# Optimization experiments

Hardware: AMD Instinct MI355X
Metric: run time of the kernel (lower is better)

Reference implementation:

```python
import jax, jax.numpy as jnp
import numpy as np

P = 3; C = 64; IMG = 48; G = IMG // P
D = C * P * P          # 576 embedding dim == flatten dim
NH = 12; HD = D // NH  # 48 head dim
HID = 4 * D            # 2304
NL = 4; S = G * G      # 256 patches
NQ = 6
QN, QP = -8.0, 7.0     # 4-bit signed LSQ range
EPS = 1e-5


def lsq(w):
    # LSQ fake-quant of weights, step size from LSQ init formula, STE rounding
    alpha = 2.0 * jnp.mean(jnp.abs(w)) / jnp.sqrt(QP)
    q = jnp.clip(w / alpha, QN, QP)
    q = q + jax.lax.stop_gradient(jnp.round(q) - q)
    return q * alpha


def qlinear(x, w, b=None):
    y = x @ lsq(w).T
    return y if b is None else y + b


def ln(x, g, b):
    m = jnp.mean(x, -1, keepdims=True)
    v = jnp.var(x, -1, keepdims=True)
    return (x - m) / jnp.sqrt(v + EPS) * g + b


def mha(q, k, v, in_w, out_w):
    # q,k,v: [S,B,D]; in_w: [3D,D]; out_w: [D,D]; no biases
    Wq, Wk, Wv = jnp.split(lsq(in_w), 3, axis=0)
    def heads(t, W):
        return (t @ W.T).reshape(t.shape[0], t.shape[1], NH, HD)
    qh = heads(q, Wq) * (1.0 / jnp.sqrt(HD))
    kh = heads(k, Wk)
    vh = heads(v, Wv)
    att = jax.nn.softmax(jnp.einsum('qbhd,kbhd->bhqk', qh, kh), axis=-1)
    o = jnp.einsum('bhqk,kbhd->qbhd', att, vh).reshape(q.shape[0], q.shape[1], D)
    return o @ lsq(out_w).T


def _forward(x, lin_enc_w, lin_enc_b, pos_emb, query_embed_w,
             enc_in_w, enc_out_w, enc_l1_w, enc_l1_b, enc_l2_w, enc_l2_b,
             enc_ln1_g, enc_ln1_b, enc_ln2_g, enc_ln2_b,
             dec_sa_in_w, dec_sa_out_w, dec_ca_in_w, dec_ca_out_w,
             dec_l1_w, dec_l1_b, dec_l2_w, dec_l2_b,
             dec_ln1_g, dec_ln1_b, dec_ln2_g, dec_ln2_b, dec_ln3_g, dec_ln3_b,
             head1_w, head1_b, head2_w, head2_b, query_idx):
    B = x.shape[0]
    # unfold -> [S,B,flat], channel-major patch flattening like F.unfold
    t = x.reshape(B, C, G, P, G, P).transpose(0, 1, 3, 5, 2, 4)
    t = t.reshape(B, C * P * P, G * G).transpose(2, 0, 1)  # [S,B,D]
    t = qlinear(t, lin_enc_w, lin_enc_b) + t
    qe = query_embed_w[query_idx].reshape(S, 1, D)   # query_pos, broadcasts over B
    pos = pos_emb[:, None, :]                        # [S,1,D]
    h = t + pos
    for l in range(NL):  # encoder (pre-norm)
        h2 = ln(h, enc_ln1_g[l], enc_ln1_b[l])
        h = h + mha(h2, h2, h2, enc_in_w[l], enc_out_w[l])
        h2 = ln(h, enc_ln2_g[l], enc_ln2_b[l])
        h = h + qlinear(jax.nn.relu(qlinear(h2, enc_l1_w[l], enc_l1_b[l])), enc_l2_w[l], enc_l2_b[l])
    mem = h
    o = mem
    for l in range(NL):  # decoder, memory = encoder output
        o2 = ln(o, dec_ln1_g[l], dec_ln1_b[l])
        qk = o2 + qe
        o = o + mha(qk, qk, o2, dec_sa_in_w[l], dec_sa_out_w[l])
        o2 = ln(o, dec_ln2_g[l], dec_ln2_b[l])
        o = o + mha(o2 + qe, mem, mem, dec_ca_in_w[l], dec_ca_out_w[l])
        o2 = ln(o, dec_ln3_g[l], dec_ln3_b[l])
        o = o + qlinear(jax.nn.relu(qlinear(o2, dec_l1_w[l], dec_l1_b[l])), dec_l2_w[l], dec_l2_b[l])
    # mlp_head with residual
    o = o + qlinear(jax.nn.relu(qlinear(o, head1_w, head1_b)), head2_w, head2_b)
    # fold back: [S,B,D] -> [B,C,IMG,IMG]
    y = o.transpose(1, 2, 0).reshape(B, C, P, P, G, G).transpose(0, 1, 4, 2, 5, 3)
    return y.reshape(B, C, IMG, IMG)


def setup_inputs() -> dict:
    key = jax.random.key(0)
    ks = iter(jax.random.split(key, 64))
    def w(shape):
        return jax.random.normal(next(ks), shape, jnp.float32) * 0.02
    B = 4
    inp = {
        'x': jax.random.normal(next(ks), (B, C, IMG, IMG), jnp.float32),
        'lin_enc_w': w((D, D)), 'lin_enc_b': jnp.zeros((D,), jnp.float32),
        'pos_emb': w((S, D)),
        'query_embed_w': w((NQ, S * D)),
        'enc_in_w': w((NL, 3 * D, D)), 'enc_out_w': w((NL, D, D)),
        'enc_l1_w': w((NL, HID, D)), 'enc_l1_b': jnp.zeros((NL, HID), jnp.float32),
        'enc_l2_w': w((NL, D, HID)), 'enc_l2_b': jnp.zeros((NL, D), jnp.float32),
        'enc_ln1_g': jnp.ones((NL, D), jnp.float32), 'enc_ln1_b': jnp.zeros((NL, D), jnp.float32),
        'enc_ln2_g': jnp.ones((NL, D), jnp.float32), 'enc_ln2_b': jnp.zeros((NL, D), jnp.float32),
        'dec_sa_in_w': w((NL, 3 * D, D)), 'dec_sa_out_w': w((NL, D, D)),
        'dec_ca_in_w': w((NL, 3 * D, D)), 'dec_ca_out_w': w((NL, D, D)),
        'dec_l1_w': w((NL, HID, D)), 'dec_l1_b': jnp.zeros((NL, HID), jnp.float32),
        'dec_l2_w': w((NL, D, HID)), 'dec_l2_b': jnp.zeros((NL, D), jnp.float32),
        'dec_ln1_g': jnp.ones((NL, D), jnp.float32), 'dec_ln1_b': jnp.zeros((NL, D), jnp.float32),
        'dec_ln2_g': jnp.ones((NL, D), jnp.float32), 'dec_ln2_b': jnp.zeros((NL, D), jnp.float32),
        'dec_ln3_g': jnp.ones((NL, D), jnp.float32), 'dec_ln3_b': jnp.zeros((NL, D), jnp.float32),
        'head1_w': w((HID, D)), 'head1_b': jnp.zeros((HID,), jnp.float32),
        'head2_w': w((D, HID)), 'head2_b': jnp.zeros((D,), jnp.float32),
        'query_idx': 0,
    }
    return inp


def reference(x, lin_enc_w, lin_enc_b, pos_emb, query_embed_w,
              enc_in_w, enc_out_w, enc_l1_w, enc_l1_b, enc_l2_w, enc_l2_b,
              enc_ln1_g, enc_ln1_b, enc_ln2_g, enc_ln2_b,
              dec_sa_in_w, dec_sa_out_w, dec_ca_in_w, dec_ca_out_w,
              dec_l1_w, dec_l1_b, dec_l2_w, dec_l2_b,
              dec_ln1_g, dec_ln1_b, dec_ln2_g, dec_ln2_b, dec_ln3_g, dec_ln3_b,
              head1_w, head1_b, head2_w, head2_b, query_idx):
    return _forward(x, lin_enc_w, lin_enc_b, pos_emb, query_embed_w,
                    enc_in_w, enc_out_w, enc_l1_w, enc_l1_b, enc_l2_w, enc_l2_b,
                    enc_ln1_g, enc_ln1_b, enc_ln2_g, enc_ln2_b,
                    dec_sa_in_w, dec_sa_out_w, dec_ca_in_w, dec_ca_out_w,
                    dec_l1_w, dec_l1_b, dec_l2_w, dec_l2_b,
                    dec_ln1_g, dec_ln1_b, dec_ln2_g, dec_ln2_b, dec_ln3_g, dec_ln3_b,
                    head1_w, head1_b, head2_w, head2_b, query_idx)
```

## Files before the change

kernel.cpp:

```cpp
#include <hip/hip_runtime.h>
#include <cstddef>

#define Pp    3
#define Cc    64
#define IMGi  48
#define Gg    16
#define Dd    576
#define NHh   12
#define HDd   48
#define HIDh  2304
#define NLl   4
#define Ss    256
#define Bb    4
#define Mm    1024
#define EPSf  1e-5f
#define NJOBS 43
#define NSTAT 20

typedef short short8 __attribute__((ext_vector_type(8)));
typedef short short4v __attribute__((ext_vector_type(4)));
typedef float f32x4  __attribute__((ext_vector_type(4)));
typedef unsigned short ushort_t;

struct QJobs { const float* ptr[NJOBS]; int n[NJOBS]; int off[NJOBS]; };

__device__ __forceinline__ short f2bf(float f) {
  unsigned u = __float_as_uint(f);
  u = u + 0x7fffu + ((u >> 16) & 1u);
  return (short)(u >> 16);
}
__device__ __forceinline__ float bf2f(short s) {
  return __uint_as_float(((unsigned)(unsigned short)s) << 16);
}

typedef __attribute__((address_space(3))) unsigned lds_u32;
typedef __attribute__((address_space(1))) const unsigned glob_u32;
__device__ __forceinline__ void gload_lds16(const void* g, void* l) {
  __builtin_amdgcn_global_load_lds((glob_u32*)g, (lds_u32*)l, 16, 0, 0);
}


__global__ void k_zero(float* p, int n) {
  int i = blockIdx.x * blockDim.x + threadIdx.x;
  if (i < n) p[i] = 0.f;
}

__global__ void k_abssum(QJobs jobs, float* absum) {
  int job = blockIdx.x >> 6, blk = blockIdx.x & 63;
  const float4* p4 = (const float4*)jobs.ptr[job];
  int n4 = jobs.n[job] >> 2;
  float s0 = 0.f, s1 = 0.f, s2 = 0.f, s3 = 0.f;
  for (int i = blk * 1024 + threadIdx.x; i < n4; i += 64 * 1024) {
    float4 v = p4[i];
    s0 += fabsf(v.x) + fabsf(v.y) + fabsf(v.z) + fabsf(v.w);
    int i1 = i + 256;
    if (i1 < n4) { float4 w = p4[i1]; s1 += fabsf(w.x) + fabsf(w.y) + fabsf(w.z) + fabsf(w.w); }
    int i2 = i + 512;
    if (i2 < n4) { float4 w = p4[i2]; s2 += fabsf(w.x) + fabsf(w.y) + fabsf(w.z) + fabsf(w.w); }
    int i3 = i + 768;
    if (i3 < n4) { float4 w = p4[i3]; s3 += fabsf(w.x) + fabsf(w.y) + fabsf(w.z) + fabsf(w.w); }
  }
  float s = (s0 + s1) + (s2 + s3);
  #pragma unroll
  for (int o = 32; o; o >>= 1) s += __shfl_xor(s, o);
  __shared__ float red[4];
  if ((threadIdx.x & 63) == 0) red[threadIdx.x >> 6] = s;
  __syncthreads();
  if (threadIdx.x == 0) atomicAdd(&absum[job], (red[0] + red[1]) + (red[2] + red[3]));
}

__global__ void k_alpha(QJobs jobs, const float* absum, float* alpha, float* inva) {
  int j = threadIdx.x;
  if (j < NJOBS) {
    float a = 2.f * (absum[j] / (float)jobs.n[j]) / sqrtf(7.f);
    alpha[j] = a;
    inva[j] = 1.f / a;
  }
}

__global__ void k_quant(QJobs jobs, const float* __restrict__ inva, short* __restrict__ wq) {
  int job = blockIdx.x >> 7, blk = blockIdx.x & 127;
  const float* p = jobs.ptr[job];
  int n8 = jobs.n[job] >> 3;
  short* dst = wq + (size_t)jobs.off[job];
  float ia = inva[job];
  for (int i = blk * 512 + threadIdx.x; i < n8; i += 128 * 512) {
    const float4* p4 = (const float4*)(p + (size_t)i * 8);
    float4 w0 = p4[0], w1 = p4[1];
    int i1 = i + 256;
    float4 w2, w3;
    bool has2 = i1 < n8;
    if (has2) { const float4* q4 = (const float4*)(p + (size_t)i1 * 8); w2 = q4[0]; w3 = q4[1]; }
    short8 bv;
    bv[0] = f2bf(rintf(fminf(7.f, fmaxf(-8.f, w0.x * ia))));
    bv[1] = f2bf(rintf(fminf(7.f, fmaxf(-8.f, w0.y * ia))));
    bv[2] = f2bf(rintf(fminf(7.f, fmaxf(-8.f, w0.z * ia))));
    bv[3] = f2bf(rintf(fminf(7.f, fmaxf(-8.f, w0.w * ia))));
    bv[4] = f2bf(rintf(fminf(7.f, fmaxf(-8.f, w1.x * ia))));
    bv[5] = f2bf(rintf(fminf(7.f, fmaxf(-8.f, w1.y * ia))));
    bv[6] = f2bf(rintf(fminf(7.f, fmaxf(-8.f, w1.z * ia))));
    bv[7] = f2bf(rintf(fminf(7.f, fmaxf(-8.f, w1.w * ia))));
    *(short8*)(dst + (size_t)i * 8) = bv;
    if (has2) {
      short8 cv;
      cv[0] = f2bf(rintf(fminf(7.f, fmaxf(-8.f, w2.x * ia))));
      cv[1] = f2bf(rintf(fminf(7.f, fmaxf(-8.f, w2.y * ia))));
      cv[2] = f2bf(rintf(fminf(7.f, fmaxf(-8.f, w2.z * ia))));
      cv[3] = f2bf(rintf(fminf(7.f, fmaxf(-8.f, w2.w * ia))));
      cv[4] = f2bf(rintf(fminf(7.f, fmaxf(-8.f, w3.x * ia))));
      cv[5] = f2bf(rintf(fminf(7.f, fmaxf(-8.f, w3.y * ia))));
      cv[6] = f2bf(rintf(fminf(7.f, fmaxf(-8.f, w3.z * ia))));
      cv[7] = f2bf(rintf(fminf(7.f, fmaxf(-8.f, w3.w * ia))));
      *(short8*)(dst + (size_t)i1 * 8) = cv;
    }
  }
}

__global__ void k_patchify(const float* __restrict__ x, float* __restrict__ t,
                           ushort_t* __restrict__ tb) {
  int i = blockIdx.x * 256 + threadIdx.x;
  if (i >= Mm * Dd) return;
  int d = i % Dd, row = i / Dd;
  int b = row % Bb, s = row / Bb;
  int c = d / 9, r = d % 9;
  int p1 = r / 3, p2 = r % 3;
  int g1 = s / Gg, g2 = s % Gg;
  float v = x[((size_t)(b * Cc + c) * IMGi + (g1 * Pp + p1)) * IMGi + (g2 * Pp + p2)];
  t[i] = v;
  tb[i] = (ushort_t)f2bf(v);
}

__global__ void k_unpatch(const float* __restrict__ h, float* __restrict__ out) {
  int i = blockIdx.x * 256 + threadIdx.x;
  if (i >= Bb * Cc * IMGi * IMGi) return;
  int j = i % IMGi, t = i / IMGi;
  int r = t % IMGi; t /= IMGi;
  int c = t % Cc;
  int b = t / Cc;
  int g1 = r / Pp, p1 = r % Pp, g2 = j / Pp, p2 = j % Pp;
  int s = g1 * Gg + g2;
  int d = c * 9 + p1 * 3 + p2;
  out[i] = h[(size_t)(s * Bb + b) * Dd + d];
}

#define MT 64
#define NT 64
#define KC 288
#define LDKB 304
#define BCHUNKS 38

__device__ __forceinline__ int bswz(int row, int colByte) {
  return row * (LDKB * 2) + (colByte ^ (((row >> 2) & 3) << 4));
}

__device__ __forceinline__ void stage_async(const ushort_t* base, int ld,
                                            char* lds, int wave, int lane) {
  #pragma unroll
  for (int j = 0; j < 10; ++j) {
    const int c = wave * 10 + j;
    if (c < BCHUNKS) {
      const int p = c * 512 + lane * 8;
      const int prow = p / LDKB;
      const int pcol2 = (p % LDKB) * 2;
      const int lcol = pcol2 ^ (((prow >> 2) & 3) << 4);
      const ushort_t* src = (lcol < 576)
        ? base + (size_t)prow * ld + (lcol >> 1)
        : base;
      gload_lds16(src, lds + c * 1024);
    }
  }
}

__global__ __launch_bounds__(256)
void k_gemm_mfma(const ushort_t* __restrict__ Xa, const ushort_t* __restrict__ Xb,
                 int n_split, int ldx,
                 const float* __restrict__ qe, const int* __restrict__ qidx,
                 const float* __restrict__ lng, const float* __restrict__ lnb,
                 const float* __restrict__ statA, const float* __restrict__ statB,
                 const float* __restrict__ Wraw, const short* __restrict__ Wq,
                 const float* __restrict__ bias, const float* __restrict__ pos,
                 const float* res, int ldr,
                 float* out, int ldo,
                 ushort_t* outbf, ushort_t* outbf2, float* statOut,
                 int N, int K,
                 const float* __restrict__ alpha_p, const float* __restrict__ inva_p,
                 int slot, int relu)
{
  __shared__ short As[NT * LDKB];
  __shared__ short Bs[NT * LDKB];
  const int tid  = threadIdx.x;
  const int wave = tid >> 6, lane = tid & 63;
  const int quad = lane >> 4, l15 = lane & 15;
  const int tile_m = blockIdx.y * MT, tile_n = blockIdx.x * NT;
  const int m_off = (wave >> 1) * 32, n_off = (wave & 1) * 32;
  const int sr = tid >> 2;
  const int sc = (tid & 3) * 8;
  const float inva = inva_p[slot];

  const bool isA = (!Xb || tile_n < n_split);
  const ushort_t* X = isA ? Xa : Xb;
  const bool addqe = (qe != nullptr) && isA;
  const float* stat = isA ? statA : statB;
  const bool a_reg = (stat != nullptr) || addqe;
  size_t qe_off = 0;
  if (addqe) qe_off = (size_t)qidx[0] * ((size_t)Ss * Dd);

  float mean = 0.f, sinv = 1.f;
  if (stat) {
    float2 st = *(const float2*)&stat[2 * (tile_m + sr)];
    mean = st.x * (1.f / (float)Dd);
    float var = st.y * (1.f / (float)Dd) - mean * mean;
    sinv = rsqrtf(var + EPSf);
  }

  f32x4 acc00 = {0,0,0,0}, acc01 = {0,0,0,0}, acc10 = {0,0,0,0}, acc11 = {0,0,0,0};

  for (int kc = 0; kc < K; kc += KC) {
    if (Wq) {
      stage_async((const ushort_t*)Wq + (size_t)tile_n * K + kc, K,
                  (char*)Bs, wave, lane);
    } else {
      const float* wr = Wraw + (size_t)(tile_n + sr) * K + kc;
      #pragma unroll
      for (int j = 0; j < 9; ++j) {
        const int k = sc + j * 32;
        float4 w0 = *(const float4*)(wr + k);
        float4 w1 = *(const float4*)(wr + k + 4);
        short8 bv;
        bv[0] = f2bf(rintf(fminf(7.f, fmaxf(-8.f, w0.x * inva))));
        bv[1] = f2bf(rintf(fminf(7.f, fmaxf(-8.f, w0.y * inva))));
        bv[2] = f2bf(rintf(fminf(7.f, fmaxf(-8.f, w0.z * inva))));
        bv[3] = f2bf(rintf(fminf(7.f, fmaxf(-8.f, w0.w * inva))));
        bv[4] = f2bf(rintf(fminf(7.f, fmaxf(-8.f, w1.x * inva))));
        bv[5] = f2bf(rintf(fminf(7.f, fmaxf(-8.f, w1.y * inva))));
        bv[6] = f2bf(rintf(fminf(7.f, fmaxf(-8.f, w1.z * inva))));
        bv[7] = f2bf(rintf(fminf(7.f, fmaxf(-8.f, w1.w * inva))));
        *(short8*)((char*)Bs + bswz(sr, k * 2)) = bv;
      }
    }

    if (!a_reg) {
      stage_async(X + (size_t)tile_m * ldx + kc, ldx, (char*)As, wave, lane);
    } else {
      const int arow = tile_m + sr;
      const ushort_t* xr = X + (size_t)arow * ldx + kc;
      const float* qr = addqe ? (qe + qe_off + (size_t)(arow >> 2) * Dd + kc) : nullptr;
      #pragma unroll
      for (int j = 0; j < 9; ++j) {
        const int k = sc + j * 32;
        short8 xv = *(const short8*)(xr + k);
        float a[8];
        #pragma unroll
        for (int e = 0; e < 8; ++e) a[e] = bf2f(xv[e]);
        if (stat) {
          float4 g0 = *(const float4*)(lng + kc + k);
          float4 g1 = *(const float4*)(lng + kc + k + 4);
          float4 b0 = *(const float4*)(lnb + kc + k);
          float4 b1 = *(const float4*)(lnb + kc + k + 4);
          a[0] = (a[0] - mean) * sinv * g0.x + b0.x;
          a[1] = (a[1] - mean) * sinv * g0.y + b0.y;
          a[2] = (a[2] - mean) * sinv * g0.z + b0.z;
          a[3] = (a[3] - mean) * sinv * g0.w + b0.w;
          a[4] = (a[4] - mean) * sinv * g1.x + b1.x;
          a[5] = (a[5] - mean) * sinv * g1.y + b1.y;
          a[6] = (a[6] - mean) * sinv * g1.z + b1.z;
          a[7] = (a[7] - mean) * sinv * g1.w + b1.w;
        }
        if (addqe) {
          float4 q0 = *(const float4*)(qr + k);
          float4 q1 = *(const float4*)(qr + k + 4);
          a[0] += q0.x; a[1] += q0.y; a[2] += q0.z; a[3] += q0.w;
          a[4] += q1.x; a[5] += q1.y; a[6] += q1.z; a[7] += q1.w;
        }
        short8 av;
        #pragma unroll
        for (int e = 0; e < 8; ++e) av[e] = f2bf(a[e]);
        *(short8*)((char*)As + bswz(sr, k * 2)) = av;
      }
    }
    __syncthreads();

    #pragma unroll 3
    for (int ks = 0; ks < KC / 32; ++ks) {
      const int kb = ks * 32 + quad * 8;
      short8 af0 = *(const short8*)((const char*)As + bswz(m_off + l15, kb * 2));
      short8 af1 = *(const short8*)((const char*)As + bswz(m_off + 16 + l15, kb * 2));
      short8 bf0 = *(const short8*)((const char*)Bs + bswz(n_off + l15, kb * 2));
      short8 bf1 = *(const short8*)((const char*)Bs + bswz(n_off + 16 + l15, kb * 2));
      acc00 = __builtin_amdgcn_mfma_f32_16x16x32_bf16(af0, bf0, acc00, 0, 0, 0);
      acc01 = __builtin_amdgcn_mfma_f32_16x16x32_bf16(af0, bf1, acc01, 0, 0, 0);
      acc10 = __builtin_amdgcn_mfma_f32_16x16x32_bf16(af1, bf0, acc10, 0, 0, 0);
      acc11 = __builtin_amdgcn_mfma_f32_16x16x32_bf16(af1, bf1, acc11, 0, 0, 0);
    }
    __syncthreads();
  }

  const float a_s = alpha_p[slot];
  const int rowb = tile_m + m_off + quad * 4;
  const int colb = tile_n + n_off + l15;
  f32x4 accs[4] = {acc00, acc01, acc10, acc11};
  float vsum[2][4], vsq[2][4];
  #pragma unroll
  for (int rt = 0; rt < 2; ++rt)
    #pragma unroll
    for (int r = 0; r < 4; ++r) { vsum[rt][r] = 0.f; vsq[rt][r] = 0.f; }

  #pragma unroll
  for (int t = 0; t < 4; ++t) {
    int row0 = rowb + ((t >> 1) * 16);
    int col  = colb + ((t & 1) * 16);
    float bv = bias ? bias[col] : 0.f;
    #pragma unroll
    for (int r = 0; r < 4; ++r) {
      int row = row0 + r;
      float v = accs[t][r] * a_s + bv;
      if (res) v += res[(size_t)row * ldr + col];
      if (pos) v += pos[(size_t)(row >> 2) * Dd + col];
      if (relu) v = fmaxf(v, 0.f);
      if (out)    out[(size_t)row * ldo + col] = v;
      if (outbf)  outbf[(size_t)row * ldo + col]  = (ushort_t)f2bf(v);
      if (outbf2) outbf2[(size_t)row * ldo + col] = (ushort_t)f2bf(v);
      vsum[t >> 1][r] += v;
      vsq[t >> 1][r]  += v * v;
    }
  }

  if (statOut) {
    #pragma unroll
    for (int rt = 0; rt < 2; ++rt) {
      #pragma unroll
      for (int r = 0; r < 4; ++r) {
        float s = vsum[rt][r], q = vsq[rt][r];
        #pragma unroll
        for (int o = 1; o < 16; o <<= 1) {
          s += __shfl_xor(s, o);
          q += __shfl_xor(q, o);
        }
        if (l15 == 0) {
          int row = rowb + rt * 16 + r;
          atomicAdd(&statOut[2 * row],     s);
          atomicAdd(&statOut[2 * row + 1], q);
        }
      }
    }
  }
}

__global__ __launch_bounds__(256)
void k_attn(const ushort_t* __restrict__ QKV, ushort_t* __restrict__ ctx, float scale) {
  __shared__ short Ks[256][72];
  __shared__ short Qs[64][72];
  __shared__ short Vt[48][264];
  __shared__ short Pq[64][264];
  const int qt = blockIdx.x;
  const int b  = blockIdx.y / NHh, h = blockIdx.y % NHh;
  const int tid = threadIdx.x;
  const int w = tid >> 6, lane = tid & 63, quad = lane >> 4, l15 = lane & 15;

  {
    const ushort_t* kp = QKV + (size_t)(tid * Bb + b) * 1728 + Dd + h * HDd;
    #pragma unroll
    for (int d0 = 0; d0 < 48; d0 += 8)
      *(short8*)&Ks[tid][d0] = *(const short8*)(kp + d0);
    short4v z = {0, 0, 0, 0};
    *(short4v*)&Ks[tid][48] = z; *(short4v*)&Ks[tid][52] = z;
    *(short4v*)&Ks[tid][56] = z; *(short4v*)&Ks[tid][60] = z;
    const ushort_t* vp = QKV + (size_t)(tid * Bb + b) * 1728 + 2 * Dd + h * HDd;
    #pragma unroll
    for (int d0 = 0; d0 < 48; d0 += 8) {
      short8 v = *(const short8*)(vp + d0);
      #pragma unroll
      for (int e = 0; e < 8; ++e) Vt[d0 + e][tid] = v[e];
    }
    if (tid < 64) {
      const ushort_t* qp = QKV + (size_t)((qt * 64 + tid) * Bb + b) * 1728 + h * HDd;
      #pragma unroll
      for (int d0 = 0; d0 < 48; d0 += 8)
        *(short8*)&Qs[tid][d0] = *(const short8*)(qp + d0);
      *(short4v*)&Qs[tid][48] = z; *(short4v*)&Qs[tid][52] = z;
      *(short4v*)&Qs[tid][56] = z; *(short4v*)&Qs[tid][60] = z;
    }
  }
  __syncthreads();

  short8 bq0 = *(short8*)&Qs[w * 16 + l15][quad * 8];
  short8 bq1 = *(short8*)&Qs[w * 16 + l15][32 + quad * 8];
  f32x4 sf[16];
  #pragma unroll
  for (int mt = 0; mt < 16; ++mt) {
    f32x4 acc = {0, 0, 0, 0};
    short8 a0 = *(short8*)&Ks[mt * 16 + l15][quad * 8];
    short8 a1 = *(short8*)&Ks[mt * 16 + l15][32 + quad * 8];
    acc = __builtin_amdgcn_mfma_f32_16x16x32_bf16(a0, bq0, acc, 0, 0, 0);
    acc = __builtin_amdgcn_mfma_f32_16x16x32_bf16(a1, bq1, acc, 0, 0, 0);
    sf[mt] = acc;
  }

  float mx = -1e30f;
  #pragma unroll
  for (int mt = 0; mt < 16; ++mt)
    #pragma unroll
    for (int r = 0; r < 4; ++r) {
      sf[mt][r] *= scale;
      mx = fmaxf(mx, sf[mt][r]);
    }
  mx = fmaxf(mx, __shfl_xor(mx, 16));
  mx = fmaxf(mx, __shfl_xor(mx, 32));
  float sum = 0.f;
  #pragma unroll
  for (int mt = 0; mt < 16; ++mt)
    #pragma unroll
    for (int r = 0; r < 4; ++r) {
      float e = __expf(sf[mt][r] - mx);
      sf[mt][r] = e;
      sum += e;
    }
  sum += __shfl_xor(sum, 16);
  sum += __shfl_xor(sum, 32);
  float inv = 1.f / sum;

  #pragma unroll
  for (int mt = 0; mt < 16; ++mt) {
    short4v p = { f2bf(sf[mt][0] * inv), f2bf(sf[mt][1] * inv),
                  f2bf(sf[mt][2] * inv), f2bf(sf[mt][3] * inv) };
    *(short4v*)&Pq[w * 16 + l15][mt * 16 + quad * 4] = p;
  }
  __syncthreads();

  f32x4 of0 = {0,0,0,0}, of1 = {0,0,0,0}, of2 = {0,0,0,0};
  #pragma unroll
  for (int kt = 0; kt < 8; ++kt) {
    short8 a = *(short8*)&Pq[w * 16 + l15][kt * 32 + quad * 8];
    short8 b0 = *(short8*)&Vt[l15][kt * 32 + quad * 8];
    short8 b1 = *(short8*)&Vt[16 + l15][kt * 32 + quad * 8];
    short8 b2 = *(short8*)&Vt[32 + l15][kt * 32 + quad * 8];
    of0 = __builtin_amdgcn_mfma_f32_16x16x32_bf16(a, b0, of0, 0, 0, 0);
    of1 = __builtin_amdgcn_mfma_f32_16x16x32_bf16(a, b1, of1, 0, 0, 0);
    of2 = __builtin_amdgcn_mfma_f32_16x16x32_bf16(a, b2, of2, 0, 0, 0);
  }
  const int qg = qt * 64 + w * 16 + quad * 4;
  #pragma unroll
  for (int r = 0; r < 4; ++r) {
    ushort_t* cr = ctx + (size_t)((qg + r) * Bb + b) * Dd + h * HDd + l15;
    cr[0]  = (ushort_t)f2bf(of0[r]);
    cr[16] = (ushort_t)f2bf(of1[r]);
    cr[32] = (ushort_t)f2bf(of2[r]);
  }
}


extern "C" void kernel_launch(void* const* d_in, const int* in_sizes, int n_in,
                              void* d_out, int out_size, void* d_ws, size_t ws_size,
                              hipStream_t stream) {
  (void)in_sizes; (void)n_in; (void)out_size;
  const float* x            = (const float*)d_in[0];
  const float* lin_enc_w    = (const float*)d_in[1];
  const float* lin_enc_b    = (const float*)d_in[2];
  const float* pos_emb      = (const float*)d_in[3];
  const float* query_embed  = (const float*)d_in[4];
  const float* enc_in_w     = (const float*)d_in[5];
  const float* enc_out_w    = (const float*)d_in[6];
  const float* enc_l1_w     = (const float*)d_in[7];
  const float* enc_l1_b     = (const float*)d_in[8];
  const float* enc_l2_w     = (const float*)d_in[9];
  const float* enc_l2_b     = (const float*)d_in[10];
  const float* enc_ln1_g    = (const float*)d_in[11];
  const float* enc_ln1_b    = (const float*)d_in[12];
  const float* enc_ln2_g    = (const float*)d_in[13];
  const float* enc_ln2_b    = (const float*)d_in[14];
  const float* dec_sa_in_w  = (const float*)d_in[15];
  const float* dec_sa_out_w = (const float*)d_in[16];
  const float* dec_ca_in_w  = (const float*)d_in[17];
  const float* dec_ca_out_w = (const float*)d_in[18];
  const float* dec_l1_w     = (const float*)d_in[19];
  const float* dec_l1_b     = (const float*)d_in[20];
  const float* dec_l2_w     = (const float*)d_in[21];
  const float* dec_l2_b     = (const float*)d_in[22];
  const float* dec_ln1_g    = (const float*)d_in[23];
  const float* dec_ln1_b    = (const float*)d_in[24];
  const float* dec_ln2_g    = (const float*)d_in[25];
  const float* dec_ln2_b    = (const float*)d_in[26];
  const float* dec_ln3_g    = (const float*)d_in[27];
  const float* dec_ln3_b    = (const float*)d_in[28];
  const float* head1_w      = (const float*)d_in[29];
  const float* head1_b      = (const float*)d_in[30];
  const float* head2_w      = (const float*)d_in[31];
  const float* head2_b      = (const float*)d_in[32];
  const int*   query_idx    = (const int*)d_in[33];
  float* out = (float*)d_out;

  const int DD  = Dd * Dd;
  const int IN3 = 3 * Dd * Dd;
  const int FF  = HIDh * Dd;
  const int MD  = Mm * Dd;

  float* ws = (float*)d_ws;
  float* ABSUM = ws;
  float* ALPHA = ws + 64;
  float* INVA  = ws + 128;
  float* STAT  = ws + 256;
  const int STATF = NSTAT * Mm * 2;
  float* H   = STAT + STATF;
  float* SCR = H + MD;
  ushort_t* Hb   = (ushort_t*)(SCR + MD);
  ushort_t* SCRb = Hb + MD;
  ushort_t* MEMb = SCRb + MD;
  ushort_t* CTXb = MEMb + MD;
  ushort_t* QKVb = CTXb + MD;
  size_t act_bytes = (256 + (size_t)STATF + 2 * (size_t)MD) * 4
                   + (4 * (size_t)MD + (size_t)Mm * HIDh) * 2;
  short* WQ = (short*)(QKVb + (size_t)Mm * HIDh);
  const size_t WQ_ELEMS = (size_t)DD + 4 * ((size_t)IN3 + DD + FF + FF)
                        + 4 * ((size_t)IN3 + DD + IN3 + DD + FF + FF)
                        + 2 * (size_t)FF;
  const bool use_wq = ws_size >= act_bytes + WQ_ELEMS * 2;

  auto T = [&](int i) { return STAT + (size_t)i * (Mm * 2); };

  QJobs jobs;
  int j = 0; int off = 0;
  auto addjob = [&](const float* p, int n) { jobs.ptr[j] = p; jobs.n[j] = n; jobs.off[j] = off; off += n; j++; };
  addjob(lin_enc_w, DD);
  for (int l = 0; l < NLl; ++l) addjob(enc_in_w  + (size_t)l * IN3, IN3);
  for (int l = 0; l < NLl; ++l) addjob(enc_out_w + (size_t)l * DD,  DD);
  for (int l = 0; l < NLl; ++l) addjob(enc_l1_w  + (size_t)l * FF,  FF);
  for (int l = 0; l < NLl; ++l) addjob(enc_l2_w  + (size_t)l * FF,  FF);
  for (int l = 0; l < NLl; ++l) addjob(dec_sa_in_w  + (size_t)l * IN3, IN3);
  for (int l = 0; l < NLl; ++l) addjob(dec_sa_out_w + (size_t)l * DD,  DD);
  for (int l = 0; l < NLl; ++l) addjob(dec_ca_in_w  + (size_t)l * IN3, IN3);
  for (int l = 0; l < NLl; ++l) addjob(dec_ca_out_w + (size_t)l * DD,  DD);
  for (int l = 0; l < NLl; ++l) addjob(dec_l1_w + (size_t)l * FF, FF);
  for (int l = 0; l < NLl; ++l) addjob(dec_l2_w + (size_t)l * FF, FF);
  addjob(head1_w, FF);
  addjob(head2_w, FF);

  const int ZN = 256 + STATF;
  k_zero<<<(ZN + 255) / 256, 256, 0, stream>>>(ws, ZN);
  k_abssum<<<NJOBS * 64, 256, 0, stream>>>(jobs, ABSUM);
  k_alpha<<<1, 64, 0, stream>>>(jobs, ABSUM, ALPHA, INVA);
  if (use_wq) k_quant<<<NJOBS * 128, 256, 0, stream>>>(jobs, INVA, WQ);

  auto gemm = [&](const ushort_t* Xa, const ushort_t* Xb, int n_split, int ldx,
                  const float* qe, const float* lng, const float* lnb,
                  const float* statA, const float* statB,
                  const float* W, int slot, const float* bias, const float* pos,
                  const float* res, int ldr,
                  float* o, int ldo, ushort_t* obf, ushort_t* obf2,
                  float* statOut, int N, int K, int relu) {
    dim3 grid(N / NT, Mm / MT);
    const short* wq = use_wq ? WQ + (size_t)jobs.off[slot] : nullptr;
    const float* wr = use_wq ? nullptr : W;
    k_gemm_mfma<<<grid, 256, 0, stream>>>(Xa, Xb, n_split, ldx, qe, query_idx,
                                          lng, lnb, statA, statB,
                                          wr, wq, bias, pos, res, ldr,
                                          o, ldo, obf, obf2, statOut,
                                          N, K, ALPHA, INVA, slot, relu);
  };

  const float scale = 1.f / sqrtf((float)HDd);
  auto attn = [&](const float* out_w, int out_slot, float* statOut) {
    k_attn<<<dim3(Ss / 64, Bb * NHh), 256, 0, stream>>>(QKVb, CTXb, scale);
    gemm(CTXb, nullptr, 0, Dd, nullptr, nullptr, nullptr, nullptr, nullptr,
         out_w, out_slot, nullptr, nullptr, H, Dd,
         H, Dd, Hb, nullptr, statOut, Dd, Dd, 0);
  };

  const int NELEM = Mm * Dd;
  const int EB = (NELEM + 255) / 256;

  k_patchify<<<EB, 256, 0, stream>>>(x, SCR, SCRb);
  gemm(SCRb, nullptr, 0, Dd, nullptr, nullptr, nullptr, nullptr, nullptr,
       lin_enc_w, 0, lin_enc_b, pos_emb, SCR, Dd,
       H, Dd, Hb, nullptr, T(0), Dd, Dd, 0);

  for (int l = 0; l < NLl; ++l) {
    gemm(Hb, nullptr, 0, Dd, nullptr, enc_ln1_g + l * Dd, enc_ln1_b + l * Dd,
         T(2 * l), nullptr,
         enc_in_w + (size_t)l * IN3, 1 + l,
         nullptr, nullptr, nullptr, 0,
         nullptr, 1728, QKVb, nullptr, nullptr, 1728, Dd, 0);
    attn(enc_out_w + (size_t)l * DD, 5 + l, T(2 * l + 1));
    gemm(Hb, nullptr, 0, Dd, nullptr, enc_ln2_g + l * Dd, enc_ln2_b + l * Dd,
         T(2 * l + 1), nullptr,
         enc_l1_w + (size_t)l * FF, 9 + l,
         enc_l1_b + l * HIDh, nullptr, nullptr, 0,
         nullptr, HIDh, QKVb, nullptr, nullptr, HIDh, Dd, 1);
    gemm(QKVb, nullptr, 0, HIDh, nullptr, nullptr, nullptr, nullptr, nullptr,
         enc_l2_w + (size_t)l * FF, 13 + l,
         enc_l2_b + l * Dd, nullptr, H, Dd,
         H, Dd, Hb, (l == NLl - 1) ? MEMb : nullptr, T(2 * l + 2),
         Dd, HIDh, 0);
  }

  for (int l = 0; l < NLl; ++l) {
    float* ln1s = T(8 + 3 * l);
    gemm(Hb, Hb, 2 * Dd, Dd, query_embed,
         dec_ln1_g + l * Dd, dec_ln1_b + l * Dd, ln1s, ln1s,
         dec_sa_in_w + (size_t)l * IN3, 17 + l,
         nullptr, nullptr, nullptr, 0,
         nullptr, 1728, QKVb, nullptr, nullptr, 1728, Dd, 0);
    attn(dec_sa_out_w + (size_t)l * DD, 21 + l, T(9 + 3 * l));
    gemm(Hb, MEMb, Dd, Dd, query_embed,
         dec_ln2_g + l * Dd, dec_ln2_b + l * Dd, T(9 + 3 * l), nullptr,
         dec_ca_in_w + (size_t)l * IN3, 25 + l,
         nullptr, nullptr, nullptr, 0,
         nullptr, 1728, QKVb, nullptr, nullptr, 1728, Dd, 0);
    attn(dec_ca_out_w + (size_t)l * DD, 29 + l, T(10 + 3 * l));
    gemm(Hb, nullptr, 0, Dd, nullptr, dec_ln3_g + l * Dd, dec_ln3_b + l * Dd,
         T(10 + 3 * l), nullptr,
         dec_l1_w + (size_t)l * FF, 33 + l,
         dec_l1_b + l * HIDh, nullptr, nullptr, 0,
         nullptr, HIDh, QKVb, nullptr, nullptr, HIDh, Dd, 1);
    gemm(QKVb, nullptr, 0, HIDh, nullptr, nullptr, nullptr, nullptr, nullptr,
         dec_l2_w + (size_t)l * FF, 37 + l,
         dec_l2_b + l * Dd, nullptr, H, Dd,
         H, Dd, Hb, nullptr, (l < NLl - 1) ? T(11 + 3 * l) : nullptr,
         Dd, HIDh, 0);
  }

  gemm(Hb, nullptr, 0, Dd, nullptr, nullptr, nullptr, nullptr, nullptr,
       head1_w, 41, head1_b, nullptr, nullptr, 0,
       nullptr, HIDh, QKVb, nullptr, nullptr, HIDh, Dd, 1);
  gemm(QKVb, nullptr, 0, HIDh, nullptr, nullptr, nullptr, nullptr, nullptr,
       head2_w, 42, head2_b, nullptr, H, Dd,
       H, Dd, nullptr, nullptr, nullptr, Dd, HIDh, 0);

  k_unpatch<<<EB, 256, 0, stream>>>(H, out);
}
```

Baseline: 1.330 ms.

## Double-buffer GEMM LDS panels for large-K and widen weight-prep kernels

```diff
diff --git a/kernel.cpp b/kernel.cpp
--- a/kernel.cpp
+++ b/kernel.cpp
@@ -46,11 +46,11 @@
 }
 
 __global__ void k_abssum(QJobs jobs, float* absum) {
-  int job = blockIdx.x >> 6, blk = blockIdx.x & 63;
+  int job = blockIdx.x >> 7, blk = blockIdx.x & 127;
   const float4* p4 = (const float4*)jobs.ptr[job];
   int n4 = jobs.n[job] >> 2;
   float s0 = 0.f, s1 = 0.f, s2 = 0.f, s3 = 0.f;
-  for (int i = blk * 1024 + threadIdx.x; i < n4; i += 64 * 1024) {
+  for (int i = blk * 1024 + threadIdx.x; i < n4; i += 128 * 1024) {
     float4 v = p4[i];
     s0 += fabsf(v.x) + fabsf(v.y) + fabsf(v.z) + fabsf(v.w);
     int i1 = i + 256;
@@ -78,41 +78,35 @@
   }
 }
 
+__device__ __forceinline__ short8 quant8(const float* p, float ia) {
+  const float4* p4 = (const float4*)p;
+  float4 w0 = p4[0], w1 = p4[1];
+  short8 bv;
+  bv[0] = f2bf(rintf(fminf(7.f, fmaxf(-8.f, w0.x * ia))));
+  bv[1] = f2bf(rintf(fminf(7.f, fmaxf(-8.f, w0.y * ia))));
+  bv[2] = f2bf(rintf(fminf(7.f, fmaxf(-8.f, w0.z * ia))));
+  bv[3] = f2bf(rintf(fminf(7.f, fmaxf(-8.f, w0.w * ia))));
+  bv[4] = f2bf(rintf(fminf(7.f, fmaxf(-8.f, w1.x * ia))));
+  bv[5] = f2bf(rintf(fminf(7.f, fmaxf(-8.f, w1.y * ia))));
+  bv[6] = f2bf(rintf(fminf(7.f, fmaxf(-8.f, w1.z * ia))));
+  bv[7] = f2bf(rintf(fminf(7.f, fmaxf(-8.f, w1.w * ia))));
+  return bv;
+}
+
 __global__ void k_quant(QJobs jobs, const float* __restrict__ inva, short* __restrict__ wq) {
   int job = blockIdx.x >> 7, blk = blockIdx.x & 127;
   const float* p = jobs.ptr[job];
   int n8 = jobs.n[job] >> 3;
   short* dst = wq + (size_t)jobs.off[job];
   float ia = inva[job];
-  for (int i = blk * 512 + threadIdx.x; i < n8; i += 128 * 512) {
-    const float4* p4 = (const float4*)(p + (size_t)i * 8);
-    float4 w0 = p4[0], w1 = p4[1];
+  for (int i = blk * 1024 + threadIdx.x; i < n8; i += 128 * 1024) {
+    *(short8*)(dst + (size_t)i * 8) = quant8(p + (size_t)i * 8, ia);
     int i1 = i + 256;
-    float4 w2, w3;
-    bool has2 = i1 < n8;
-    if (has2) { const float4* q4 = (const float4*)(p + (size_t)i1 * 8); w2 = q4[0]; w3 = q4[1]; }
-    short8 bv;
-    bv[0] = f2bf(rintf(fminf(7.f, fmaxf(-8.f, w0.x * ia))));
-    bv[1] = f2bf(rintf(fminf(7.f, fmaxf(-8.f, w0.y * ia))));
-    bv[2] = f2bf(rintf(fminf(7.f, fmaxf(-8.f, w0.z * ia))));
-    bv[3] = f2bf(rintf(fminf(7.f, fmaxf(-8.f, w0.w * ia))));
-    bv[4] = f2bf(rintf(fminf(7.f, fmaxf(-8.f, w1.x * ia))));
-    bv[5] = f2bf(rintf(fminf(7.f, fmaxf(-8.f, w1.y * ia))));
-    bv[6] = f2bf(rintf(fminf(7.f, fmaxf(-8.f, w1.z * ia))));
-    bv[7] = f2bf(rintf(fminf(7.f, fmaxf(-8.f, w1.w * ia))));
-    *(short8*)(dst + (size_t)i * 8) = bv;
-    if (has2) {
-      short8 cv;
-      cv[0] = f2bf(rintf(fminf(7.f, fmaxf(-8.f, w2.x * ia))));
-      cv[1] = f2bf(rintf(fminf(7.f, fmaxf(-8.f, w2.y * ia))));
-      cv[2] = f2bf(rintf(fminf(7.f, fmaxf(-8.f, w2.z * ia))));
-      cv[3] = f2bf(rintf(fminf(7.f, fmaxf(-8.f, w2.w * ia))));
-      cv[4] = f2bf(rintf(fminf(7.f, fmaxf(-8.f, w3.x * ia))));
-      cv[5] = f2bf(rintf(fminf(7.f, fmaxf(-8.f, w3.y * ia))));
-      cv[6] = f2bf(rintf(fminf(7.f, fmaxf(-8.f, w3.z * ia))));
-      cv[7] = f2bf(rintf(fminf(7.f, fmaxf(-8.f, w3.w * ia))));
-      *(short8*)(dst + (size_t)i1 * 8) = cv;
-    }
+    if (i1 < n8) *(short8*)(dst + (size_t)i1 * 8) = quant8(p + (size_t)i1 * 8, ia);
+    int i2 = i + 512;
+    if (i2 < n8) *(short8*)(dst + (size_t)i2 * 8) = quant8(p + (size_t)i2 * 8, ia);
+    int i3 = i + 768;
+    if (i3 < n8) *(short8*)(dst + (size_t)i3 * 8) = quant8(p + (size_t)i3 * 8, ia);
   }
 }
 
@@ -147,6 +141,7 @@
 #define NT 64
 #define KC 288
 #define LDKB 304
+#define PANEL (NT * LDKB)
 #define BCHUNKS 38
 
 __device__ __forceinline__ int bswz(int row, int colByte) {
@@ -171,6 +166,7 @@
   }
 }
 
+template <int DB>
 __global__ __launch_bounds__(256)
 void k_gemm_mfma(const ushort_t* __restrict__ Xa, const ushort_t* __restrict__ Xb,
                  int n_split, int ldx,
@@ -186,8 +182,8 @@
                  const float* __restrict__ alpha_p, const float* __restrict__ inva_p,
                  int slot, int relu)
 {
-  __shared__ short As[NT * LDKB];
-  __shared__ short Bs[NT * LDKB];
+  __shared__ short As[DB * PANEL];
+  __shared__ short Bs[DB * PANEL];
   const int tid  = threadIdx.x;
   const int wave = tid >> 6, lane = tid & 63;
   const int quad = lane >> 4, l15 = lane & 15;
@@ -215,32 +211,24 @@
 
   f32x4 acc00 = {0,0,0,0}, acc01 = {0,0,0,0}, acc10 = {0,0,0,0}, acc11 = {0,0,0,0};
 
-  for (int kc = 0; kc < K; kc += KC) {
+  auto STAGE = [&](int kc, int buf) {
+    short* Asb = As + buf * PANEL;
+    short* Bsb = Bs + buf * PANEL;
     if (Wq) {
       stage_async((const ushort_t*)Wq + (size_t)tile_n * K + kc, K,
-                  (char*)Bs, wave, lane);
+                  (char*)Bsb, wave, lane);
     } else {
       const float* wr = Wraw + (size_t)(tile_n + sr) * K + kc;
       #pragma unroll
       for (int j = 0; j < 9; ++j) {
         const int k = sc + j * 32;
-        float4 w0 = *(const float4*)(wr + k);
-        float4 w1 = *(const float4*)(wr + k + 4);
         short8 bv;
-        bv[0] = f2bf(rintf(fminf(7.f, fmaxf(-8.f, w0.x * inva))));
-        bv[1] = f2bf(rintf(fminf(7.f, fmaxf(-8.f, w0.y * inva))));
-        bv[2] = f2bf(rintf(fminf(7.f, fmaxf(-8.f, w0.z * inva))));
-        bv[3] = f2bf(rintf(fminf(7.f, fmaxf(-8.f, w0.w * inva))));
-        bv[4] = f2bf(rintf(fminf(7.f, fmaxf(-8.f, w1.x * inva))));
-        bv[5] = f2bf(rintf(fminf(7.f, fmaxf(-8.f, w1.y * inva))));
-        bv[6] = f2bf(rintf(fminf(7.f, fmaxf(-8.f, w1.z * inva))));
-        bv[7] = f2bf(rintf(fminf(7.f, fmaxf(-8.f, w1.w * inva))));
-        *(short8*)((char*)Bs + bswz(sr, k * 2)) = bv;
+        bv = quant8(wr + k, inva);
+        *(short8*)((char*)Bsb + bswz(sr, k * 2)) = bv;
       }
     }
-
     if (!a_reg) {
-      stage_async(X + (size_t)tile_m * ldx + kc, ldx, (char*)As, wave, lane);
+      stage_async(X + (size_t)tile_m * ldx + kc, ldx, (char*)Asb, wave, lane);
     } else {
       const int arow = tile_m + sr;
       const ushort_t* xr = X + (size_t)arow * ldx + kc;
@@ -275,24 +263,44 @@
         short8 av;
         #pragma unroll
         for (int e = 0; e < 8; ++e) av[e] = f2bf(a[e]);
-        *(short8*)((char*)As + bswz(sr, k * 2)) = av;
+        *(short8*)((char*)Asb + bswz(sr, k * 2)) = av;
       }
     }
-    __syncthreads();
-
+  };
+
+  auto COMPUTE = [&](int buf) {
+    const short* Asb = As + buf * PANEL;
+    const short* Bsb = Bs + buf * PANEL;
     #pragma unroll 3
     for (int ks = 0; ks < KC / 32; ++ks) {
       const int kb = ks * 32 + quad * 8;
-      short8 af0 = *(const short8*)((const char*)As + bswz(m_off + l15, kb * 2));
-      short8 af1 = *(const short8*)((const char*)As + bswz(m_off + 16 + l15, kb * 2));
-      short8 bf0 = *(const short8*)((const char*)Bs + bswz(n_off + l15, kb * 2));
-      short8 bf1 = *(const short8*)((const char*)Bs + bswz(n_off + 16 + l15, kb * 2));
+      short8 af0 = *(const short8*)((const char*)Asb + bswz(m_off + l15, kb * 2));
+      short8 af1 = *(const short8*)((const char*)Asb + bswz(m_off + 16 + l15, kb * 2));
+      short8 bf0 = *(const short8*)((const char*)Bsb + bswz(n_off + l15, kb * 2));
+      short8 bf1 = *(const short8*)((const char*)Bsb + bswz(n_off + 16 + l15, kb * 2));
       acc00 = __builtin_amdgcn_mfma_f32_16x16x32_bf16(af0, bf0, acc00, 0, 0, 0);
       acc01 = __builtin_amdgcn_mfma_f32_16x16x32_bf16(af0, bf1, acc01, 0, 0, 0);
       acc10 = __builtin_amdgcn_mfma_f32_16x16x32_bf16(af1, bf0, acc10, 0, 0, 0);
       acc11 = __builtin_amdgcn_mfma_f32_16x16x32_bf16(af1, bf1, acc11, 0, 0, 0);
     }
+  };
+
+  const int nc = K / KC;
+  if (DB == 2) {
+    STAGE(0, 0);
     __syncthreads();
+    for (int c = 0; c < nc; ++c) {
+      if (c + 1 < nc) STAGE((c + 1) * KC, (c + 1) & 1);
+      COMPUTE(c & 1);
+      __syncthreads();
+    }
+  } else {
+    for (int c = 0; c < nc; ++c) {
+      STAGE(c * KC, 0);
+      __syncthreads();
+      COMPUTE(0);
+      __syncthreads();
+    }
   }
 
   const float a_s = alpha_p[slot];
@@ -536,7 +544,7 @@
 
   const int ZN = 256 + STATF;
   k_zero<<<(ZN + 255) / 256, 256, 0, stream>>>(ws, ZN);
-  k_abssum<<<NJOBS * 64, 256, 0, stream>>>(jobs, ABSUM);
+  k_abssum<<<NJOBS * 128, 256, 0, stream>>>(jobs, ABSUM);
   k_alpha<<<1, 64, 0, stream>>>(jobs, ABSUM, ALPHA, INVA);
   if (use_wq) k_quant<<<NJOBS * 128, 256, 0, stream>>>(jobs, INVA, WQ);
 
@@ -550,11 +558,18 @@
     dim3 grid(N / NT, Mm / MT);
     const short* wq = use_wq ? WQ + (size_t)jobs.off[slot] : nullptr;
     const float* wr = use_wq ? nullptr : W;
-    k_gemm_mfma<<<grid, 256, 0, stream>>>(Xa, Xb, n_split, ldx, qe, query_idx,
-                                          lng, lnb, statA, statB,
-                                          wr, wq, bias, pos, res, ldr,
-                                          o, ldo, obf, obf2, statOut,
-                                          N, K, ALPHA, INVA, slot, relu);
+    if (K > 2 * KC)
+      k_gemm_mfma<2><<<grid, 256, 0, stream>>>(Xa, Xb, n_split, ldx, qe, query_idx,
+                                               lng, lnb, statA, statB,
+                                               wr, wq, bias, pos, res, ldr,
+                                               o, ldo, obf, obf2, statOut,
+                                               N, K, ALPHA, INVA, slot, relu);
+    else
+      k_gemm_mfma<1><<<grid, 256, 0, stream>>>(Xa, Xb, n_split, ldx, qe, query_idx,
+                                               lng, lnb, statA, statB,
+                                               wr, wq, bias, pos, res, ldr,
+                                               o, ldo, obf, obf2, statOut,
+                                               N, K, ALPHA, INVA, slot, relu);
   };
 
   const float scale = 1.f / sqrtf((float)HDd);
```

Measured after the change: 1.316 ms. Within noise of the previous version (-1.1%).
